# Kernel tuning notes

Hardware: AMD Instinct MI355X
Metric: run time of the kernel (lower is better)

## Reference

```python
import jax, jax.numpy as jnp
import numpy as np

B, T, D = 4, 2048, 1024
H, DH, E, SEL = 8, 64, 5, 2


def setup_inputs() -> dict:
    key = jax.random.key(0)
    ks = jax.random.split(key, 7)
    s = 0.02
    x = jax.random.normal(ks[0], (B, T, D), dtype=jnp.float32)
    Wq = jax.random.normal(ks[1], (D, H * DH), dtype=jnp.float32) * s
    Wk = jax.random.normal(ks[2], (D, H * DH), dtype=jnp.float32) * s
    Ws = jax.random.normal(ks[3], (D, H * E), dtype=jnp.float32) * s   # gate for V experts
    Wd = jax.random.normal(ks[4], (D, H * E), dtype=jnp.float32) * s   # gate for out experts
    Wv = jax.random.normal(ks[5], (E, D, DH), dtype=jnp.float32) * s   # experts_v weights
    Wo = jax.random.normal(ks[6], (E, DH, D), dtype=jnp.float32) * s   # experts_out weights
    return {"x": x, "Wq": Wq, "Wk": Wk, "Ws": Ws, "Wd": Wd, "Wv": Wv, "Wo": Wo}


def _topk_mask(logits, k):
    # 0/1 mask of top-k experts along last axis (torch.topk indices are distinct)
    _, idx = jax.lax.top_k(logits, k)
    return jnp.sum(jax.nn.one_hot(idx, logits.shape[-1], dtype=logits.dtype), axis=-2)


def reference(x, Wq, Wk, Ws, Wd, Wv, Wo):
    e, d, dh = Wv.shape
    h = Wq.shape[1] // dh
    b, t, _ = x.shape
    scale = dh ** -0.5

    q = (x @ Wq).reshape(b, t, h, dh).transpose(0, 2, 1, 3)  # b h t d
    k = (x @ Wk).reshape(b, t, h, dh).transpose(0, 2, 1, 3)  # b h t d

    # moe_v: per-(b,t,head) top-k experts, sigmoid-weighted combine of expert V projections
    gl_v = (x @ Ws).reshape(b, t, h, e)                      # b t h e
    wv = _topk_mask(gl_v, SEL) * jax.nn.sigmoid(gl_v)        # b t h e (zero off selected)
    xv = jnp.einsum('btd,edk->btek', x, Wv)                  # all-expert V: b t e dh
    v = jnp.einsum('bthe,btek->bhtk', wv, xv)                # b h t dh

    scores = jnp.einsum('bhid,bhjd->bhij', q * scale, k)     # b h t t
    probs = jax.nn.softmax(scores, axis=-1)
    attn = jnp.einsum('bhij,bhjd->bihd', probs, v)           # b t h dh

    # moe_out: top-k selection (weights computed but unused in original), unweighted sum,
    # then sum over heads — fuse both reductions into one einsum
    gl_o = (x @ Wd).reshape(b, t, h, e)
    mask_o = _topk_mask(gl_o, SEL)                           # b t h e
    out = jnp.einsum('bthe,bthk,ekd->btd', mask_o, attn, Wo)  # b t d
    return out
```

## Files before the change

### kernel.cpp

```cpp
#include <hip/hip_runtime.h>
#include <cstdint>
#include <cstddef>

#define BB 4
#define TT 2048
#define DD 1024
#define HH 8
#define DH 64
#define EE 5
#define MM (BB*TT)
#define PLD 1344
#define NWT 1408

typedef short short8 __attribute__((ext_vector_type(8)));
typedef float f32x4  __attribute__((ext_vector_type(4)));
typedef float f32x16 __attribute__((ext_vector_type(16)));
typedef unsigned int u32x2 __attribute__((ext_vector_type(2)));

__device__ __forceinline__ float bflo(uint32_t u) { union { uint32_t i; float f; } v; v.i = u << 16; return v.f; }
__device__ __forceinline__ float bfhi(uint32_t u) { union { uint32_t i; float f; } v; v.i = u & 0xFFFF0000u; return v.f; }
__device__ __forceinline__ float bf2f(uint16_t u) { union { uint32_t i; float f; } v; v.i = ((uint32_t)u) << 16; return v.f; }
__device__ __forceinline__ uint32_t pkbf(float a, float b) {
  uint32_t ua = __float_as_uint(a) + 0x8000u;
  uint32_t ub = __float_as_uint(b) + 0x8000u;
  return __builtin_amdgcn_perm(ub, ua, 0x07060302u);
}
__device__ __forceinline__ uint16_t bfr1(float f) {
  return (uint16_t)((__float_as_uint(f) + 0x8000u) >> 16);
}
__device__ __forceinline__ uint32_t cvtpk(float a, float b) {
  uint32_t r;
  asm("v_cvt_pk_bf16_f32 %0, %1, %2" : "=v"(r) : "v"(a), "v"(b));
  return r;
}

__device__ __forceinline__ void gload16(const void* g, void* l) {
  __builtin_amdgcn_global_load_lds(
      (const __attribute__((address_space(1))) uint32_t*)g,
      (__attribute__((address_space(3))) uint32_t*)l, 16, 0, 0);
}

__global__ __launch_bounds__(256) void pack_wt_kernel(
    const float* __restrict__ Wq, const float* __restrict__ Wk,
    const float* __restrict__ Wv, uint16_t* __restrict__ Wt)
{
  __shared__ __align__(16) uint16_t Ts[64 * 68];
  int k0 = blockIdx.x * 64, n0 = blockIdx.y * 64;
  int t = threadIdx.x;
#pragma unroll
  for (int rep = 0; rep < 16; ++rep) {
    int li = rep * 256 + t;
    int kl = li >> 6, nl = li & 63;
    int k = k0 + kl, n = n0 + nl;
    float v = 0.f;
    if (n < 512)       v = Wq[k * 512 + n];
    else if (n < 1024) v = Wk[k * 512 + (n - 512)];
    else if (n < 1344) { int nn = n - 1024; v = Wv[((size_t)(nn >> 6) * 1024 + k) * 64 + (nn & 63)]; }
    Ts[kl * 68 + nl] = bfr1(v);
  }
  __syncthreads();
#pragma unroll
  for (int rep = 0; rep < 16; ++rep) {
    int li = rep * 256 + t;
    int nl = li >> 6, kl = li & 63;
    Wt[(size_t)(n0 + nl) * 1024 + k0 + kl] = Ts[kl * 68 + nl];
  }
}

__global__ __launch_bounds__(256) void pack_wot_kernel(
    const float* __restrict__ Wo, uint16_t* __restrict__ WoT)
{
  __shared__ __align__(16) uint16_t Ts[64 * 68];
  int k0 = blockIdx.x * 64, n0 = blockIdx.y * 64;
  int t = threadIdx.x;
#pragma unroll
  for (int rep = 0; rep < 16; ++rep) {
    int li = rep * 256 + t;
    int kl = li >> 6, nl = li & 63;
    Ts[kl * 68 + nl] = bfr1(Wo[(size_t)(k0 + kl) * 1024 + n0 + nl]);
  }
  __syncthreads();
#pragma unroll
  for (int rep = 0; rep < 16; ++rep) {
    int li = rep * 256 + t;
    int nl = li >> 6, kl = li & 63;
    WoT[(size_t)(n0 + nl) * 320 + k0 + kl] = Ts[kl * 68 + nl];
  }
}

__global__ __launch_bounds__(256) void xbf_kernel(const float* __restrict__ x, uint16_t* __restrict__ xb)
{
  int i = (blockIdx.x * 256 + threadIdx.x) * 4;
  float4 v = *(const float4*)(x + i);
  uint2 o;
  o.x = pkbf(v.x, v.y);
  o.y = pkbf(v.z, v.w);
  *(uint2*)(xb + i) = o;
}

__device__ __forceinline__ void top2_5(float g0, float g1, float g2, float g3, float g4,
                                       int& i1, float& b1, int& i2, float& b2) {
  i1 = 0; b1 = g0;
  if (g1 > b1) { b1 = g1; i1 = 1; }
  if (g2 > b1) { b1 = g2; i1 = 2; }
  if (g3 > b1) { b1 = g3; i1 = 3; }
  if (g4 > b1) { b1 = g4; i1 = 4; }
  i2 = -1; b2 = -__builtin_inff();
  if (i1 != 0 && g0 > b2) { b2 = g0; i2 = 0; }
  if (i1 != 1 && g1 > b2) { b2 = g1; i2 = 1; }
  if (i1 != 2 && g2 > b2) { b2 = g2; i2 = 2; }
  if (i1 != 3 && g3 > b2) { b2 = g3; i2 = 3; }
  if (i1 != 4 && g4 > b2) { b2 = g4; i2 = 4; }
}

__device__ __forceinline__ void ldw20(float* d, const float* __restrict__ p) {
#pragma unroll
  for (int j = 0; j < 20; ++j) d[j] = p[j];
}
__device__ __forceinline__ void fma20(float* acc, const float* wv, float xv) {
#pragma unroll
  for (int j = 0; j < 20; ++j) acc[j] = fmaf(xv, wv[j], acc[j]);
}

__global__ __launch_bounds__(1024) void gate_v6_kernel(
    const float* __restrict__ x, const float* __restrict__ Ws,
    const float* __restrict__ Wd, uint32_t* __restrict__ gsel32)
{
  __shared__ __align__(16) float xs[10752];
  int t = threadIdx.x;
  int m0 = blockIdx.x * 64;
  int g  = blockIdx.y;
  int w = t >> 6, lane = t & 63;
  int cg = __builtin_amdgcn_readfirstlane(w & 1);
  int kq = __builtin_amdgcn_readfirstlane(w >> 1);
  const float* __restrict__ Wg = g ? Wd : Ws;
  const float* __restrict__ wbase = Wg + (size_t)(kq * 16) * 40 + cg * 20;

  float acc[20];
#pragma unroll
  for (int j = 0; j < 20; ++j) acc[j] = 0.f;

  for (int tile = 0; tile < 8; ++tile) {
    __syncthreads();
#pragma unroll
    for (int rep = 0; rep < 2; ++rep) {
      int li = rep * 1024 + t;
      int row = li >> 5, kg = li & 31;
      float4 v = *(const float4*)&x[(size_t)(m0 + row) * 1024 + tile * 128 + kg * 4];
      *(float4*)&xs[row * 132 + kg * 4] = v;
    }
    __syncthreads();

    const float* wp = wbase + (size_t)tile * 128 * 40;
    const float* xp = &xs[lane * 132 + kq * 16];
    float wc[20], wn[20];
    ldw20(wc, wp);
#pragma unroll
    for (int k4 = 0; k4 < 4; ++k4) {
      float4 xv = *(const float4*)&xp[k4 * 4];
      ldw20(wn, wp + (size_t)(k4 * 4 + 1) * 40);
      fma20(acc, wc, xv.x);
      ldw20(wc, wp + (size_t)(k4 * 4 + 2) * 40);
      fma20(acc, wn, xv.y);
      ldw20(wn, wp + (size_t)(k4 * 4 + 3) * 40);
      fma20(acc, wc, xv.z);
      if (k4 < 3) ldw20(wc, wp + (size_t)(k4 * 4 + 4) * 40);
      fma20(acc, wn, xv.w);
    }
  }

  float* red = xs;
  __syncthreads();
  if (kq & 1) {
    int ro = (((kq >> 1) * 2 + cg) * 64 + lane) * 21;
#pragma unroll
    for (int j = 0; j < 20; ++j) red[ro + j] = acc[j];
  }
  __syncthreads();
  if (!(kq & 1)) {
    int ro = (((kq >> 1) * 2 + cg) * 64 + lane) * 21;
#pragma unroll
    for (int j = 0; j < 20; ++j) acc[j] += red[ro + j];
  }
  __syncthreads();
  if (kq == 2 || kq == 6) {
    int ro = (((kq >> 2) * 2 + cg) * 64 + lane) * 21;
#pragma unroll
    for (int j = 0; j < 20; ++j) red[ro + j] = acc[j];
  }
  __syncthreads();
  if (kq == 0 || kq == 4) {
    int ro = (((kq >> 2) * 2 + cg) * 64 + lane) * 21;
#pragma unroll
    for (int j = 0; j < 20; ++j) acc[j] += red[ro + j];
  }
  __syncthreads();
  if (kq == 4) {
    int ro = (cg * 64 + lane) * 21;
#pragma unroll
    for (int j = 0; j < 20; ++j) red[ro + j] = acc[j];
  }
  __syncthreads();

  if (kq == 0) {
    int ro = (cg * 64 + lane) * 21;
#pragma unroll
    for (int j = 0; j < 20; ++j) acc[j] += red[ro + j];
    int m = m0 + lane;
    if (g == 0) {
#pragma unroll
      for (int hh = 0; hh < 4; ++hh) {
        int i1, i2; float b1, b2;
        top2_5(acc[hh * 5 + 0], acc[hh * 5 + 1], acc[hh * 5 + 2],
               acc[hh * 5 + 3], acc[hh * 5 + 4], i1, b1, i2, b2);
        float w1 = 1.f / (1.f + __expf(-b1));
        float w2 = 1.f / (1.f + __expf(-b2));
        uint32_t* gp = gsel32 + ((size_t)m * 8 + cg * 4 + hh) * 4;
        gp[0] = __float_as_uint(w1);
        gp[1] = __float_as_uint(w2);
        gp[2] = (uint32_t)(i1 | (i2 << 3));
      }
    } else {
#pragma unroll
      for (int hh = 0; hh < 4; ++hh) {
        int j1, j2; float c1, c2;
        top2_5(acc[hh * 5 + 0], acc[hh * 5 + 1], acc[hh * 5 + 2],
               acc[hh * 5 + 3], acc[hh * 5 + 4], j1, c1, j2, c2);
        uint32_t* gp = gsel32 + ((size_t)m * 8 + cg * 4 + hh) * 4;
        gp[3] = (uint32_t)(j1 | (j2 << 3));
      }
    }
  }
}

__global__ __launch_bounds__(256) void proj_mfma_kernel(
    const uint16_t* __restrict__ xb, const uint16_t* __restrict__ Wt,
    uint16_t* __restrict__ proj)
{
  __shared__ __align__(16) uint16_t As[128 * 32];
  __shared__ __align__(16) uint16_t Bs[128 * 32];
  int t = threadIdx.x;
  int n0 = blockIdx.x * 128, m0 = blockIdx.y * 128;
  int w = t >> 6, lane = t & 63, q = lane >> 4, c = lane & 15;
  int wm = w & 1, wn = w >> 1;
  int lr = lane >> 2, lc = (lane & 3) * 8;
  f32x4 zf = {0.f, 0.f, 0.f, 0.f};
  f32x4 acc[4][4];
#pragma unroll
  for (int i = 0; i < 4; ++i)
#pragma unroll
    for (int j = 0; j < 4; ++j) acc[i][j] = zf;

  for (int kb = 0; kb < 32; ++kb) {
    __syncthreads();
#pragma unroll
    for (int j = 0; j < 2; ++j) {
      int row = w * 32 + j * 16 + lr;
      gload16(xb + (size_t)(m0 + row) * 1024 + kb * 32 + lc,
              &As[(w * 32 + j * 16) * 32 + lane * 8]);
      gload16(Wt + (size_t)(n0 + row) * 1024 + kb * 32 + lc,
              &Bs[(w * 32 + j * 16) * 32 + lane * 8]);
    }
    __syncthreads();
    short8 af[4], bfr[4];
#pragma unroll
    for (int i = 0; i < 4; ++i)
      af[i] = *(const short8*)&As[(wm * 64 + i * 16 + c) * 32 + q * 8];
#pragma unroll
    for (int j = 0; j < 4; ++j)
      bfr[j] = *(const short8*)&Bs[(wn * 64 + j * 16 + c) * 32 + q * 8];
#pragma unroll
    for (int i = 0; i < 4; ++i)
#pragma unroll
      for (int j = 0; j < 4; ++j)
        acc[i][j] = __builtin_amdgcn_mfma_f32_16x16x32_bf16(af[i], bfr[j], acc[i][j], 0, 0, 0);
  }
#pragma unroll
  for (int i = 0; i < 4; ++i)
#pragma unroll
    for (int j = 0; j < 4; ++j) {
      int col = n0 + wn * 64 + j * 16 + c;
      if (col < PLD) {
#pragma unroll
        for (int reg = 0; reg < 4; ++reg) {
          int row = m0 + wm * 64 + i * 16 + q * 4 + reg;
          proj[(size_t)row * PLD + col] = bfr1(acc[i][j][reg]);
        }
      }
    }
}

__global__ __launch_bounds__(256) void out_mfma_kernel(
    const uint16_t* __restrict__ zb, const uint16_t* __restrict__ WoT,
    float* __restrict__ out)
{
  __shared__ __align__(16) uint16_t As[128 * 32];
  __shared__ __align__(16) uint16_t Bs[128 * 32];
  int t = threadIdx.x;
  int n0 = blockIdx.x * 128, m0 = blockIdx.y * 128;
  int w = t >> 6, lane = t & 63, q = lane >> 4, c = lane & 15;
  int wm = w & 1, wn = w >> 1;
  int lr = lane >> 2, lc = (lane & 3) * 8;
  f32x4 zf = {0.f, 0.f, 0.f, 0.f};
  f32x4 acc[4][4];
#pragma unroll
  for (int i = 0; i < 4; ++i)
#pragma unroll
    for (int j = 0; j < 4; ++j) acc[i][j] = zf;

  for (int kb = 0; kb < 10; ++kb) {
    __syncthreads();
#pragma unroll
    for (int j = 0; j < 2; ++j) {
      int row = w * 32 + j * 16 + lr;
      gload16(zb + (size_t)(m0 + row) * 320 + kb * 32 + lc,
              &As[(w * 32 + j * 16) * 32 + lane * 8]);
      gload16(WoT + (size_t)(n0 + row) * 320 + kb * 32 + lc,
              &Bs[(w * 32 + j * 16) * 32 + lane * 8]);
    }
    __syncthreads();
    short8 af[4], bfr[4];
#pragma unroll
    for (int i = 0; i < 4; ++i)
      af[i] = *(const short8*)&As[(wm * 64 + i * 16 + c) * 32 + q * 8];
#pragma unroll
    for (int j = 0; j < 4; ++j)
      bfr[j] = *(const short8*)&Bs[(wn * 64 + j * 16 + c) * 32 + q * 8];
#pragma unroll
    for (int i = 0; i < 4; ++i)
#pragma unroll
      for (int j = 0; j < 4; ++j)
        acc[i][j] = __builtin_amdgcn_mfma_f32_16x16x32_bf16(af[i], bfr[j], acc[i][j], 0, 0, 0);
  }
#pragma unroll
  for (int i = 0; i < 4; ++i)
#pragma unroll
    for (int j = 0; j < 4; ++j) {
      int col = n0 + wn * 64 + j * 16 + c;
#pragma unroll
      for (int reg = 0; reg < 4; ++reg) {
        int row = m0 + wm * 64 + i * 16 + q * 4 + reg;
        out[(size_t)row * 1024 + col] = acc[i][j][reg];
      }
    }
}

__global__ __launch_bounds__(256) void vbuild_kernel(
    const uint16_t* __restrict__ proj, const uint4* __restrict__ gsel,
    uint16_t* __restrict__ vt)
{
  int bi = blockIdx.x;
  int bh = bi >> 5, tb = bi & 31;
  int b = bh >> 3, h = bh & 7;
  int t = threadIdx.x;
  int tt = t & 63, dg = t >> 6;
  int m = b * 2048 + tb * 64 + tt;
  uint4 gs = gsel[m * 8 + h];
  float w1 = __uint_as_float(gs.x), w2 = __uint_as_float(gs.y);
  int i1 = gs.z & 7, i2 = (gs.z >> 3) & 7;
  const uint16_t* base = proj + (size_t)m * PLD + 1024;
  const uint4* p1 = (const uint4*)(base + i1 * 64 + dg * 16);
  const uint4* p2 = (const uint4*)(base + i2 * 64 + dg * 16);
  uint4 A0 = p1[0], A1 = p1[1], B0 = p2[0], B1 = p2[1];
  float v[16];
  v[0]  = w1*bflo(A0.x) + w2*bflo(B0.x); v[1]  = w1*bfhi(A0.x) + w2*bfhi(B0.x);
  v[2]  = w1*bflo(A0.y) + w2*bflo(B0.y); v[3]  = w1*bfhi(A0.y) + w2*bfhi(B0.y);
  v[4]  = w1*bflo(A0.z) + w2*bflo(B0.z); v[5]  = w1*bfhi(A0.z) + w2*bfhi(B0.z);
  v[6]  = w1*bflo(A0.w) + w2*bflo(B0.w); v[7]  = w1*bfhi(A0.w) + w2*bfhi(B0.w);
  v[8]  = w1*bflo(A1.x) + w2*bflo(B1.x); v[9]  = w1*bfhi(A1.x) + w2*bfhi(B1.x);
  v[10] = w1*bflo(A1.y) + w2*bflo(B1.y); v[11] = w1*bfhi(A1.y) + w2*bfhi(B1.y);
  v[12] = w1*bflo(A1.z) + w2*bflo(B1.z); v[13] = w1*bfhi(A1.z) + w2*bfhi(B1.z);
  v[14] = w1*bflo(A1.w) + w2*bflo(B1.w); v[15] = w1*bfhi(A1.w) + w2*bfhi(B1.w);
#pragma unroll
  for (int dd = 0; dd < 16; ++dd)
    vt[(size_t)(bh * 64 + dg * 16 + dd) * 2048 + tb * 64 + tt] = bfr1(v[dd]);
}

__global__ __launch_bounds__(256) void flash_mfma_kernel(
    const uint16_t* __restrict__ proj, const uint16_t* __restrict__ vt,
    uint16_t* __restrict__ attnb)
{
  __shared__ __align__(16) uint16_t Ks[64 * 72];
  __shared__ __align__(16) uint16_t Vs[64 * 72];
  __shared__ float lsb[4 * 32];
  int t = threadIdx.x;
  int bx = blockIdx.x;
  int qb = bx & 15, bh = bx >> 4;
  int h = bh & 7, b = bh >> 3;
  int w = t >> 6, lane = t & 63;
  int r31 = lane & 31, hi = lane >> 5;
  int srow = t >> 2, scq = t & 3;

  short8 qf[4];
  {
    const uint16_t* qp = proj + (size_t)(b * 2048 + qb * 128 + w * 32 + r31) * PLD + h * 64 + hi * 8;
#pragma unroll
    for (int f = 0; f < 4; ++f) qf[f] = *(const short8*)(qp + 16 * f);
  }

  f32x16 o0 = {0.f}, o1 = {0.f};
#pragma unroll
  for (int i = 0; i < 16; ++i) { o0[i] = 0.f; o1[i] = 0.f; }
  float lsacc = 0.f;

  const uint16_t* kg = proj + (size_t)(b * 2048 + srow) * PLD + 512 + h * 64 + scq * 16;
  const uint16_t* vg = vt + (size_t)(bh * 64 + srow) * 2048 + scq * 16;
  uint4 kp0, kp1, vp0, vp1;
  kp0 = ((const uint4*)kg)[0]; kp1 = ((const uint4*)kg)[1];
  vp0 = ((const uint4*)vg)[0]; vp1 = ((const uint4*)vg)[1];

  for (int it = 0; it < 32; ++it) {
    if (it) __syncthreads();
    *(uint4*)&Ks[srow * 72 + scq * 16] = kp0;
    *(uint4*)&Ks[srow * 72 + scq * 16 + 8] = kp1;
    *(uint4*)&Vs[srow * 72 + scq * 16] = vp0;
    *(uint4*)&Vs[srow * 72 + scq * 16 + 8] = vp1;
    __syncthreads();
    if (it < 31) {
      const uint4* pk = (const uint4*)(kg + (size_t)(it + 1) * 64 * PLD);
      kp0 = pk[0]; kp1 = pk[1];
      const uint4* pv = (const uint4*)(vg + (it + 1) * 64);
      vp0 = pv[0]; vp1 = pv[1];
    }

    short8 pa[4];
#pragma unroll
    for (int jg = 0; jg < 2; ++jg) {
      f32x16 s;
#pragma unroll
      for (int i = 0; i < 16; ++i) s[i] = 0.f;
#pragma unroll
      for (int f = 0; f < 4; ++f) {
        short8 kf = *(const short8*)&Ks[(jg * 32 + r31) * 72 + hi * 8 + 16 * f];
        s = __builtin_amdgcn_mfma_f32_32x32x16_bf16(kf, qf[f], s, 0, 0, 0);
      }
      float p[16];
#pragma unroll
      for (int reg = 0; reg < 16; ++reg)
        p[reg] = __builtin_amdgcn_exp2f(s[reg] * 0.18033688f);
      lsacc += (((p[0] + p[1]) + (p[2] + p[3])) + ((p[4] + p[5]) + (p[6] + p[7])))
             + (((p[8] + p[9]) + (p[10] + p[11])) + ((p[12] + p[13]) + (p[14] + p[15])));
      uint32_t X1 = cvtpk(p[0], p[1]),  X2 = cvtpk(p[2], p[3]);
      uint32_t Y1 = cvtpk(p[4], p[5]),  Y2 = cvtpk(p[6], p[7]);
      uint32_t Z1 = cvtpk(p[8], p[9]),  Z2 = cvtpk(p[10], p[11]);
      uint32_t W1 = cvtpk(p[12], p[13]), W2 = cvtpk(p[14], p[15]);
      u32x2 s1 = __builtin_amdgcn_permlane32_swap(X1, Y1, false, false);
      u32x2 s2 = __builtin_amdgcn_permlane32_swap(X2, Y2, false, false);
      u32x2 s3 = __builtin_amdgcn_permlane32_swap(Z1, W1, false, false);
      u32x2 s4 = __builtin_amdgcn_permlane32_swap(Z2, W2, false, false);
      uint4 f0 = { s1.x, s2.x, s1.y, s2.y };
      uint4 f1 = { s3.x, s4.x, s3.y, s4.y };
      pa[jg * 2 + 0] = *(short8*)&f0;
      pa[jg * 2 + 1] = *(short8*)&f1;
    }

#pragma unroll
    for (int f = 0; f < 4; ++f) {
      short8 vf0 = *(const short8*)&Vs[(r31) * 72 + hi * 8 + 16 * f];
      short8 vf1 = *(const short8*)&Vs[(32 + r31) * 72 + hi * 8 + 16 * f];
      o0 = __builtin_amdgcn_mfma_f32_32x32x16_bf16(pa[f], vf0, o0, 0, 0, 0);
      o1 = __builtin_amdgcn_mfma_f32_32x32x16_bf16(pa[f], vf1, o1, 0, 0, 0);
    }
  }

  float lsc = lsacc + __shfl_xor(lsacc, 32);
  if (lane < 32) lsb[w * 32 + r31] = 1.0f / lsc;
#pragma unroll
  for (int reg = 0; reg < 16; ++reg) {
    int r = (reg & 3) + 8 * (reg >> 2) + 4 * hi;
    float inv = lsb[w * 32 + r];
    size_t row = (size_t)(b * 2048 + qb * 128 + w * 32 + r);
    attnb[row * 512 + h * 64 + r31]      = bfr1(o0[reg] * inv);
    attnb[row * 512 + h * 64 + 32 + r31] = bfr1(o1[reg] * inv);
  }
}

__global__ __launch_bounds__(64) void zbuild_kernel(
    const uint16_t* __restrict__ attnb, const uint32_t* __restrict__ gselw,
    uint16_t* __restrict__ zbuf)
{
  int m = blockIdx.x; int c = threadIdx.x;
  float acc[5] = {0.f, 0.f, 0.f, 0.f, 0.f};
#pragma unroll
  for (int h = 0; h < 8; ++h) {
    uint32_t sel = gselw[(m * 8 + h) * 4 + 3];
    int e1 = sel & 7, e2 = (sel >> 3) & 7;
    float a = bf2f(attnb[(size_t)m * 512 + h * 64 + c]);
#pragma unroll
    for (int e = 0; e < 5; ++e)
      acc[e] += (e == e1 || e == e2) ? a : 0.f;
  }
#pragma unroll
  for (int e = 0; e < 5; ++e)
    zbuf[(size_t)m * 320 + e * 64 + c] = bfr1(acc[e]);
}

extern "C" void kernel_launch(void* const* d_in, const int* in_sizes, int n_in,
                              void* d_out, int out_size, void* d_ws, size_t ws_size,
                              hipStream_t stream) {
  const float* x  = (const float*)d_in[0];
  const float* Wq = (const float*)d_in[1];
  const float* Wk = (const float*)d_in[2];
  const float* Ws = (const float*)d_in[3];
  const float* Wd = (const float*)d_in[4];
  const float* Wv = (const float*)d_in[5];
  const float* Wo = (const float*)d_in[6];
  float* out = (float*)d_out;

  char* ws = (char*)d_ws;
  uint4*    gsel  = (uint4*)   (ws);
  uint16_t* WoT   = (uint16_t*)(ws + 1048576);
  uint16_t* Wt    = (uint16_t*)(ws + 1703936);
  uint16_t* xb    = (uint16_t*)(ws + 4587520);
  uint16_t* proj  = (uint16_t*)(ws + 21364736);
  uint16_t* vt    = (uint16_t*)(ws + 43384832);
  uint16_t* attnb = (uint16_t*)(ws + 1703936);
  uint16_t* zbuf  = (uint16_t*)(ws + 10092544);

  gate_v6_kernel<<<dim3(MM / 64, 2), 1024, 0, stream>>>(x, Ws, Wd, (uint32_t*)gsel);
  pack_wt_kernel<<<dim3(16, 22), 256, 0, stream>>>(Wq, Wk, Wv, Wt);
  pack_wot_kernel<<<dim3(5, 16), 256, 0, stream>>>(Wo, WoT);
  xbf_kernel<<<(MM * DD / 4) / 256, 256, 0, stream>>>(x, xb);
  proj_mfma_kernel<<<dim3(NWT / 128, MM / 128), 256, 0, stream>>>(xb, Wt, proj);
  vbuild_kernel<<<32 * 32, 256, 0, stream>>>(proj, gsel, vt);
  flash_mfma_kernel<<<BB * HH * (TT / 128), 256, 0, stream>>>(proj, vt, attnb);
  zbuild_kernel<<<MM, 64, 0, stream>>>(attnb, (const uint32_t*)gsel, zbuf);
  out_mfma_kernel<<<dim3(DD / 128, MM / 128), 256, 0, stream>>>(zbuf, WoT, out);
}
```

Before: 239.7 us.

## Split flash attention KV range across two warp groups per block

The flash attention kernel now launches 512 threads per block. Two groups of four waves each process half of the key/value sequence with separate shared-memory tiles. Their partial outputs and softmax denominators are then reduced through shared memory before the final write. This doubles the parallelism per query block to raise occupancy and latency hiding on the 512-block grid, at the cost of an extra shared-memory exchange, more LDS per block, and half of the threads sitting idle during the epilogue.

```diff
diff --git a/kernel.cpp b/kernel.cpp
--- a/kernel.cpp
+++ b/kernel.cpp
@@ -376,24 +376,28 @@
     vt[(size_t)(bh * 64 + dg * 16 + dd) * 2048 + tb * 64 + tt] = bfr1(v[dd]);
 }
 
-__global__ __launch_bounds__(256) void flash_mfma_kernel(
+__global__ __launch_bounds__(512) void flash_mfma_kernel(
     const uint16_t* __restrict__ proj, const uint16_t* __restrict__ vt,
     uint16_t* __restrict__ attnb)
 {
-  __shared__ __align__(16) uint16_t Ks[64 * 72];
-  __shared__ __align__(16) uint16_t Vs[64 * 72];
-  __shared__ float lsb[4 * 32];
+  __shared__ __align__(16) char smem[36864];
   int t = threadIdx.x;
   int bx = blockIdx.x;
   int qb = bx & 15, bh = bx >> 4;
   int h = bh & 7, b = bh >> 3;
-  int w = t >> 6, lane = t & 63;
+  int g = t >> 8;
+  int tg = t & 255;
+  int w = t >> 6, wl = w & 3;
+  int lane = t & 63;
   int r31 = lane & 31, hi = lane >> 5;
-  int srow = t >> 2, scq = t & 3;
+  int srow = tg >> 2, scq = tg & 3;
+
+  uint16_t* Ksg = (uint16_t*)smem + g * 4608;
+  uint16_t* Vsg = (uint16_t*)smem + 9216 + g * 4608;
 
   short8 qf[4];
   {
-    const uint16_t* qp = proj + (size_t)(b * 2048 + qb * 128 + w * 32 + r31) * PLD + h * 64 + hi * 8;
+    const uint16_t* qp = proj + (size_t)(b * 2048 + qb * 128 + wl * 32 + r31) * PLD + h * 64 + hi * 8;
 #pragma unroll
     for (int f = 0; f < 4; ++f) qf[f] = *(const short8*)(qp + 16 * f);
   }
@@ -403,20 +407,20 @@
   for (int i = 0; i < 16; ++i) { o0[i] = 0.f; o1[i] = 0.f; }
   float lsacc = 0.f;
 
-  const uint16_t* kg = proj + (size_t)(b * 2048 + srow) * PLD + 512 + h * 64 + scq * 16;
-  const uint16_t* vg = vt + (size_t)(bh * 64 + srow) * 2048 + scq * 16;
+  const uint16_t* kg = proj + (size_t)(b * 2048 + g * 1024 + srow) * PLD + 512 + h * 64 + scq * 16;
+  const uint16_t* vg = vt + (size_t)(bh * 64 + srow) * 2048 + g * 1024 + scq * 16;
   uint4 kp0, kp1, vp0, vp1;
   kp0 = ((const uint4*)kg)[0]; kp1 = ((const uint4*)kg)[1];
   vp0 = ((const uint4*)vg)[0]; vp1 = ((const uint4*)vg)[1];
 
-  for (int it = 0; it < 32; ++it) {
+  for (int it = 0; it < 16; ++it) {
     if (it) __syncthreads();
-    *(uint4*)&Ks[srow * 72 + scq * 16] = kp0;
-    *(uint4*)&Ks[srow * 72 + scq * 16 + 8] = kp1;
-    *(uint4*)&Vs[srow * 72 + scq * 16] = vp0;
-    *(uint4*)&Vs[srow * 72 + scq * 16 + 8] = vp1;
-    __syncthreads();
-    if (it < 31) {
+    *(uint4*)&Ksg[srow * 72 + scq * 16] = kp0;
+    *(uint4*)&Ksg[srow * 72 + scq * 16 + 8] = kp1;
+    *(uint4*)&Vsg[srow * 72 + scq * 16] = vp0;
+    *(uint4*)&Vsg[srow * 72 + scq * 16 + 8] = vp1;
+    __syncthreads();
+    if (it < 15) {
       const uint4* pk = (const uint4*)(kg + (size_t)(it + 1) * 64 * PLD);
       kp0 = pk[0]; kp1 = pk[1];
       const uint4* pv = (const uint4*)(vg + (it + 1) * 64);
@@ -431,7 +435,7 @@
       for (int i = 0; i < 16; ++i) s[i] = 0.f;
 #pragma unroll
       for (int f = 0; f < 4; ++f) {
-        short8 kf = *(const short8*)&Ks[(jg * 32 + r31) * 72 + hi * 8 + 16 * f];
+        short8 kf = *(const short8*)&Ksg[(jg * 32 + r31) * 72 + hi * 8 + 16 * f];
         s = __builtin_amdgcn_mfma_f32_32x32x16_bf16(kf, qf[f], s, 0, 0, 0);
       }
       float p[16];
@@ -456,22 +460,45 @@
 
 #pragma unroll
     for (int f = 0; f < 4; ++f) {
-      short8 vf0 = *(const short8*)&Vs[(r31) * 72 + hi * 8 + 16 * f];
-      short8 vf1 = *(const short8*)&Vs[(32 + r31) * 72 + hi * 8 + 16 * f];
+      short8 vf0 = *(const short8*)&Vsg[(r31) * 72 + hi * 8 + 16 * f];
+      short8 vf1 = *(const short8*)&Vsg[(32 + r31) * 72 + hi * 8 + 16 * f];
       o0 = __builtin_amdgcn_mfma_f32_32x32x16_bf16(pa[f], vf0, o0, 0, 0, 0);
       o1 = __builtin_amdgcn_mfma_f32_32x32x16_bf16(pa[f], vf1, o1, 0, 0, 0);
     }
   }
 
   float lsc = lsacc + __shfl_xor(lsacc, 32);
-  if (lane < 32) lsb[w * 32 + r31] = 1.0f / lsc;
-#pragma unroll
-  for (int reg = 0; reg < 16; ++reg) {
-    int r = (reg & 3) + 8 * (reg >> 2) + 4 * hi;
-    float inv = lsb[w * 32 + r];
-    size_t row = (size_t)(b * 2048 + qb * 128 + w * 32 + r);
-    attnb[row * 512 + h * 64 + r31]      = bfr1(o0[reg] * inv);
-    attnb[row * 512 + h * 64 + 32 + r31] = bfr1(o1[reg] * inv);
+  __syncthreads();
+  float* xch = (float*)smem;
+  float* xls = (float*)(smem + 33792);
+  float* lsb = (float*)(smem + 34304);
+  if (g == 1) {
+    int base = (wl * 64 + lane) * 33;
+#pragma unroll
+    for (int reg = 0; reg < 16; ++reg) {
+      xch[base + reg] = o0[reg];
+      xch[base + 16 + reg] = o1[reg];
+    }
+    if (lane < 32) xls[wl * 32 + r31] = lsc;
+  }
+  __syncthreads();
+  if (g == 0) {
+    int base = (wl * 64 + lane) * 33;
+#pragma unroll
+    for (int reg = 0; reg < 16; ++reg) {
+      o0[reg] += xch[base + reg];
+      o1[reg] += xch[base + 16 + reg];
+    }
+    float lst = lsc + xls[wl * 32 + r31];
+    if (lane < 32) lsb[wl * 32 + r31] = 1.0f / lst;
+#pragma unroll
+    for (int reg = 0; reg < 16; ++reg) {
+      int r = (reg & 3) + 8 * (reg >> 2) + 4 * hi;
+      float inv = lsb[wl * 32 + r];
+      size_t row = (size_t)(b * 2048 + qb * 128 + wl * 32 + r);
+      attnb[row * 512 + h * 64 + r31]      = bfr1(o0[reg] * inv);
+      attnb[row * 512 + h * 64 + 32 + r31] = bfr1(o1[reg] * inv);
+    }
   }
 }
 
@@ -523,7 +550,7 @@
   xbf_kernel<<<(MM * DD / 4) / 256, 256, 0, stream>>>(x, xb);
   proj_mfma_kernel<<<dim3(NWT / 128, MM / 128), 256, 0, stream>>>(xb, Wt, proj);
   vbuild_kernel<<<32 * 32, 256, 0, stream>>>(proj, gsel, vt);
-  flash_mfma_kernel<<<BB * HH * (TT / 128), 256, 0, stream>>>(proj, vt, attnb);
+  flash_mfma_kernel<<<BB * HH * (TT / 128), 512, 0, stream>>>(proj, vt, attnb);
   zbuild_kernel<<<MM, 64, 0, stream>>>(attnb, (const uint32_t*)gsel, zbuf);
   out_mfma_kernel<<<dim3(DD / 128, MM / 128), 256, 0, stream>>>(zbuf, WoT, out);
 }
```

Measured after the change: 236.5 us. Within noise of the previous version (-1.3%).
